# Optimization experiments

Measured on AMD Instinct MI355X. Metric: run time of the kernel, lower is better.

Reference implementation:

```python
import jax, jax.numpy as jnp
import numpy as np

NUM_HEADS = 16
HEAD_DIM = 128
MODEL_DIM = 2048
SEQ = 4096
INIT = 0.02


def setup_inputs() -> dict:
    key = jax.random.key(0)
    k1, k2, k3 = jax.random.split(key, 3)
    x = jax.random.normal(k1, (SEQ, MODEL_DIM), dtype=jnp.float32)
    w_attn = jax.random.normal(k2, (MODEL_DIM, 3 * MODEL_DIM), dtype=jnp.float32) * INIT
    b_attn = jnp.zeros((3 * MODEL_DIM,), dtype=jnp.float32)
    w_proj = jax.random.normal(k3, (MODEL_DIM, MODEL_DIM), dtype=jnp.float32) * INIT
    b_proj = jnp.zeros((MODEL_DIM,), dtype=jnp.float32)
    return {"x": x, "w_attn": w_attn, "b_attn": b_attn, "w_proj": w_proj, "b_proj": b_proj}


def reference(x, w_attn, b_attn, w_proj, b_proj):
    seq = x.shape[0]
    # fused QKV projection: [seq, 3*model_dim]
    hidden = x @ w_attn + b_attn
    q, k, v = jnp.split(hidden, 3, axis=-1)
    q = q.reshape(seq, NUM_HEADS, HEAD_DIM)
    k = k.reshape(seq, NUM_HEADS, HEAD_DIM)
    v = v.reshape(seq, NUM_HEADS, HEAD_DIM)
    q = q / jnp.sqrt(jnp.asarray(HEAD_DIM, dtype=q.dtype))
    # scores: [heads, q, k]
    scores = jnp.einsum('qhd,khd->hqk', q, k)
    causal = jnp.tril(jnp.ones((seq, seq), dtype=bool))  # mask[q, k]
    big_neg = jnp.finfo(jnp.float32).min
    scores = jnp.where(causal[None, :, :], scores, big_neg)
    pattern = jax.nn.softmax(scores, axis=-1)
    z = jnp.einsum('hqk,khd->qhd', pattern, v)
    out = z.reshape(seq, MODEL_DIM) @ w_proj + b_proj
    return out
```

## Files before the change

### kernel.cpp

```cpp
#include <hip/hip_runtime.h>
#include <hip/hip_bf16.h>
#include <stdint.h>
#include <stddef.h>

typedef __bf16 bf16_8 __attribute__((ext_vector_type(8)));
typedef __bf16 bf16_4 __attribute__((ext_vector_type(4)));
typedef float f32x4 __attribute__((ext_vector_type(4)));

#define BIG_NEG (-1e30f)
#define QSCALE (0.08838834764831845f * 1.4426950408889634f)
#define FIXMAX 16.0f

__device__ __forceinline__ void gld_lds16(const void* g, void* l) {
  __builtin_amdgcn_global_load_lds(
      (const __attribute__((address_space(1))) uint32_t*)g,
      (__attribute__((address_space(3))) uint32_t*)l, 16, 0, 0);
}

#define BAR()                      \
  do {                             \
    asm volatile("" ::: "memory"); \
    __builtin_amdgcn_s_barrier();  \
    asm volatile("" ::: "memory"); \
  } while (0)

__global__ __launch_bounds__(256) void convert_bf16(
    const float* __restrict__ in, __bf16* __restrict__ out, long long n) {
  long long i = ((long long)blockIdx.x * 256 + threadIdx.x) * 8;
  if (i + 8 > n) return;
  const float4* in4 = (const float4*)(in + i);
  float4 a = in4[0], b = in4[1];
  bf16_8 o = {(__bf16)a.x, (__bf16)a.y, (__bf16)a.z, (__bf16)a.w,
              (__bf16)b.x, (__bf16)b.y, (__bf16)b.z, (__bf16)b.w};
  *(bf16_8*)(out + i) = o;
}

__global__ __launch_bounds__(256) void transpose_cvt(
    const float* __restrict__ in, __bf16* __restrict__ out, int R, int C) {
  __shared__ __bf16 tile[32][33];
  int bx = blockIdx.x * 32;
  int by = blockIdx.y * 32;
  int tx = threadIdx.x;
  int ty = threadIdx.y;
#pragma unroll
  for (int j = 0; j < 32; j += 8)
    tile[ty + j][tx] = (__bf16)in[(size_t)(by + ty + j) * C + bx + tx];
  __syncthreads();
#pragma unroll
  for (int j = 0; j < 32; j += 8)
    out[(size_t)(bx + ty + j) * R + by + tx] = tile[tx][ty + j];
}

__global__ __launch_bounds__(512, 2) void gemm_bt256(
    const __bf16* __restrict__ A, const __bf16* __restrict__ Bt,
    const float* __restrict__ bias, __bf16* __restrict__ C0,
    __bf16* __restrict__ VT, float* __restrict__ Cf,
    int M, int N, int K, int mode) {
  __shared__ __bf16 As[2][128 * 64];
  __shared__ __bf16 Bs[2][256 * 64];

  const int t = threadIdx.x;
  const int lane = t & 63;
  const int wave = t >> 6;
  const int col = lane & 15;
  const int quad = lane >> 4;
  const int wr = wave >> 2;
  const int wc = wave & 3;
  const int m0 = blockIdx.y * 128;
  const int n0 = blockIdx.x * 256;
  const bool vswap = (mode == 1) && (n0 >= 4096);

  const int trow = t >> 3;
  const int sk = (((trow & 7) ^ (t & 7)) * 8);
  const __bf16* gA = A + (size_t)(m0 + trow) * K + sk;
  const __bf16* gB = Bt + (size_t)(n0 + trow) * K + sk;
  const int ldst = wave * 512;

  const int ar = wr * 64 + col;
  const int br = wc * 64 + col;
  const int sq0 = ((quad) ^ (col & 7)) * 8;
  const int sq1 = ((quad ^ 4) ^ (col & 7)) * 8;

  f32x4 acc[4][4];
#pragma unroll
  for (int i = 0; i < 4; i++)
#pragma unroll
    for (int j = 0; j < 4; j++) acc[i][j] = f32x4{0.f, 0.f, 0.f, 0.f};

  const int nk = K / 64;

#define STA(b, L, kk) \
  gld_lds16(gA + (size_t)(L) * 64 * K + (kk), &As[b][(L) * 4096 + ldst])
#define STB(b, L, kk) \
  gld_lds16(gB + (size_t)(L) * 64 * K + (kk), &Bs[b][(L) * 4096 + ldst])

#define RDA(c)                                                         \
  do {                                                                 \
    afp[0] = *(const bf16_8*)(&As[cb][(ar + (c) * 16) * 64 + sq0]);    \
    afp[1] = *(const bf16_8*)(&As[cb][(ar + (c) * 16) * 64 + sq1]);    \
  } while (0)

#define CL(c)                                                          \
  do {                                                                 \
    if (!vswap) {                                                      \
      _Pragma("unroll") for (int ni = 0; ni < 4; ++ni) {               \
        acc[(c)][ni] = __builtin_amdgcn_mfma_f32_16x16x32_bf16(        \
            afp[0], bfr[ni][0], acc[(c)][ni], 0, 0, 0);                \
        acc[(c)][ni] = __builtin_amdgcn_mfma_f32_16x16x32_bf16(        \
            afp[1], bfr[ni][1], acc[(c)][ni], 0, 0, 0);                \
      }                                                                \
    } else {                                                           \
      _Pragma("unroll") for (int ni = 0; ni < 4; ++ni) {               \
        acc[(c)][ni] = __builtin_amdgcn_mfma_f32_16x16x32_bf16(        \
            bfr[ni][0], afp[0], acc[(c)][ni], 0, 0, 0);                \
        acc[(c)][ni] = __builtin_amdgcn_mfma_f32_16x16x32_bf16(        \
            bfr[ni][1], afp[1], acc[(c)][ni], 0, 0, 0);                \
      }                                                                \
    }                                                                  \
  } while (0)

#define LGKM0()                                       \
  do {                                                \
    asm volatile("s_waitcnt lgkmcnt(0)" ::: "memory");\
    __builtin_amdgcn_sched_barrier(0);                \
  } while (0)

  STA(0, 0, 0); STA(0, 1, 0);
  STB(0, 0, 0); STB(0, 1, 0); STB(0, 2, 0); STB(0, 3, 0);
  STA(1, 0, 64); STA(1, 1, 64);
  STB(1, 0, 64); STB(1, 1, 64); STB(1, 2, 64); STB(1, 3, 64);
  asm volatile("s_waitcnt vmcnt(6)" ::: "memory");
  BAR();

  for (int kt = 0; kt < nk; ++kt) {
    const int cb = kt & 1;
    const int kk = (kt + 2) * 64;
    const bool st = (kt + 2) < nk;

    bf16_8 bfr[4][2], afp[2];
#pragma unroll
    for (int ni = 0; ni < 4; ++ni) {
      bfr[ni][0] = *(const bf16_8*)(&Bs[cb][(br + ni * 16) * 64 + sq0]);
      bfr[ni][1] = *(const bf16_8*)(&Bs[cb][(br + ni * 16) * 64 + sq1]);
    }
    RDA(0);
    LGKM0();
    __builtin_amdgcn_s_setprio(1);
    CL(0);
    __builtin_amdgcn_s_setprio(0);

    BAR();
    if (st) { STB(cb, 0, kk); STB(cb, 1, kk); STB(cb, 2, kk); STB(cb, 3, kk); }

    RDA(1);
    LGKM0();
    __builtin_amdgcn_s_setprio(1);
    CL(1);
    __builtin_amdgcn_s_setprio(0);

    RDA(2);
    LGKM0();
    __builtin_amdgcn_s_setprio(1);
    CL(2);
    __builtin_amdgcn_s_setprio(0);

    RDA(3);
    LGKM0();
    BAR();
    if (st) { STA(cb, 0, kk); STA(cb, 1, kk); }
    __builtin_amdgcn_sched_barrier(0);
    __builtin_amdgcn_s_setprio(1);
    CL(3);
    __builtin_amdgcn_s_setprio(0);

    if (st)
      asm volatile("s_waitcnt vmcnt(6)" ::: "memory");
    else
      asm volatile("s_waitcnt vmcnt(0)" ::: "memory");
    BAR();
  }
#undef STA
#undef STB
#undef RDA
#undef CL
#undef LGKM0

  if (mode == 0) {
#pragma unroll
    for (int mi = 0; mi < 4; mi++)
#pragma unroll
      for (int ni = 0; ni < 4; ni++) {
        int gn = n0 + wc * 64 + ni * 16 + col;
        float bv = bias[gn];
#pragma unroll
        for (int r = 0; r < 4; r++)
          Cf[(size_t)(m0 + wr * 64 + mi * 16 + quad * 4 + r) * N + gn] =
              acc[mi][ni][r] + bv;
      }
  } else if (n0 < 2048) {
#pragma unroll
    for (int mi = 0; mi < 4; mi++)
#pragma unroll
      for (int ni = 0; ni < 4; ni++) {
        int gn = n0 + wc * 64 + ni * 16 + col;
        float bv = bias[gn];
#pragma unroll
        for (int r = 0; r < 4; r++)
          C0[(size_t)(m0 + wr * 64 + mi * 16 + quad * 4 + r) * 4096 + gn] =
              (__bf16)((acc[mi][ni][r] + bv) * QSCALE);
      }
  } else if (n0 < 4096) {
#pragma unroll
    for (int mi = 0; mi < 4; mi++)
#pragma unroll
      for (int ni = 0; ni < 4; ni++) {
        int gn = n0 + wc * 64 + ni * 16 + col;
        float bv = bias[gn];
#pragma unroll
        for (int r = 0; r < 4; r++)
          C0[(size_t)(m0 + wr * 64 + mi * 16 + quad * 4 + r) * 4096 + gn] =
              (__bf16)(acc[mi][ni][r] + bv);
      }
  } else {
#pragma unroll
    for (int mi = 0; mi < 4; mi++) {
      int seq = m0 + wr * 64 + mi * 16 + col;
#pragma unroll
      for (int ni = 0; ni < 4; ni++) {
#pragma unroll
        for (int r = 0; r < 4; r++) {
          int gn = n0 + wc * 64 + ni * 16 + quad * 4 + r;
          float bv = bias[gn];
          VT[(size_t)(gn - 4096) * M + seq] = (__bf16)(acc[mi][ni][r] + bv);
        }
      }
    }
  }
}

__global__ __launch_bounds__(256, 2) void flash_attn(
    const __bf16* __restrict__ QK, const __bf16* __restrict__ VT,
    __bf16* __restrict__ Z) {
  constexpr int KS = 136;
  constexpr int VS = 72;
  constexpr int PS = 72;
  __shared__ __bf16 Ks[64 * KS];
  __shared__ __bf16 Vs[128 * VS];
  __shared__ __bf16 Ps[4 * 2 * 16 * PS];

  const int t = threadIdx.x;
  const int lane = t & 63;
  const int wave = t >> 6;
  const int col = lane & 15;
  const int quad = lane >> 4;
  const int h = blockIdx.y;
  const int ta = 31 - blockIdx.x;
  const int q0 = ta * 128;
  const int nkb = 2 * (ta + 1);

  const __bf16* kbase =
      QK + (size_t)(t >> 4) * 4096 + 2048 + h * 128 + (t & 15) * 8;
  __bf16* kdst = Ks + (t >> 4) * KS + (t & 15) * 8;
  const __bf16* vbase = VT + (size_t)(h * 128 + (t >> 3)) * 4096 + (t & 7) * 8;
  __bf16* vdst = Vs + (t >> 3) * VS + (t & 7) * 8;

  bf16_8 qf[4][2];
  {
#pragma unroll
    for (int qg = 0; qg < 2; qg++) {
      const __bf16* qp =
          QK + (size_t)(q0 + wave * 32 + qg * 16 + col) * 4096 + h * 128;
#pragma unroll
      for (int i = 0; i < 4; i++)
        qf[i][qg] = *(const bf16_8*)(qp + i * 32 + quad * 8);
    }
  }

  f32x4 z[8][2];
#pragma unroll
  for (int i = 0; i < 8; i++) {
    z[i][0] = f32x4{0.f, 0.f, 0.f, 0.f};
    z[i][1] = f32x4{0.f, 0.f, 0.f, 0.f};
  }
  float lsum[2] = {0.f, 0.f};

  bf16_8 kpre[4], vpre[4];
#pragma unroll
  for (int j = 0; j < 4; j++) {
    kpre[j] = *(const bf16_8*)(kbase + (size_t)j * 16 * 4096);
    vpre[j] = *(const bf16_8*)(vbase + (size_t)j * 32 * 4096);
  }

  __bf16* pw0 = Ps + (wave * 2 + 0) * 16 * PS;
  __bf16* pw1 = Ps + (wave * 2 + 1) * 16 * PS;

  for (int kb = 0; kb < nkb; kb++) {
    const int k0 = kb * 64;
    __syncthreads();
#pragma unroll
    for (int j = 0; j < 4; j++) {
      *(bf16_8*)(kdst + j * 16 * KS) = kpre[j];
      *(bf16_8*)(vdst + j * 32 * VS) = vpre[j];
    }
    __syncthreads();

    if (kb + 1 < nkb) {
      const __bf16* kb2 = kbase + (size_t)(k0 + 64) * 4096;
      const __bf16* vb2 = vbase + (k0 + 64);
#pragma unroll
      for (int j = 0; j < 4; j++) {
        kpre[j] = *(const bf16_8*)(kb2 + (size_t)j * 16 * 4096);
        vpre[j] = *(const bf16_8*)(vb2 + (size_t)j * 32 * 4096);
      }
    }

    f32x4 sh[4][2];
    __builtin_amdgcn_s_setprio(1);
#pragma unroll
    for (int p = 0; p < 4; p++) {
      sh[p][0] = f32x4{0.f, 0.f, 0.f, 0.f};
      sh[p][1] = f32x4{0.f, 0.f, 0.f, 0.f};
#pragma unroll
      for (int kd = 0; kd < 4; kd++) {
        bf16_8 kf =
            *(const bf16_8*)(Ks + (p * 16 + col) * KS + kd * 32 + quad * 8);
        sh[p][0] = __builtin_amdgcn_mfma_f32_16x16x32_bf16(kf, qf[kd][0],
                                                           sh[p][0], 0, 0, 0);
        sh[p][1] = __builtin_amdgcn_mfma_f32_16x16x32_bf16(kf, qf[kd][1],
                                                           sh[p][1], 0, 0, 0);
      }
    }
    __builtin_amdgcn_s_setprio(0);

    if (kb >= nkb - 2) {
#pragma unroll
      for (int qg = 0; qg < 2; qg++) {
        int qgl = q0 + wave * 32 + qg * 16 + col;
#pragma unroll
        for (int p = 0; p < 4; p++)
#pragma unroll
          for (int r = 0; r < 4; r++)
            if (k0 + p * 16 + quad * 4 + r > qgl) sh[p][qg][r] = BIG_NEG;
      }
    }

#pragma unroll
    for (int qg = 0; qg < 2; qg++) {
      __bf16* pw = qg ? pw1 : pw0;
      float rs = 0.f;
#pragma unroll
      for (int p = 0; p < 4; p++) {
        float e0 = exp2f(sh[p][qg][0] - FIXMAX);
        float e1 = exp2f(sh[p][qg][1] - FIXMAX);
        float e2 = exp2f(sh[p][qg][2] - FIXMAX);
        float e3 = exp2f(sh[p][qg][3] - FIXMAX);
        rs += (e0 + e1) + (e2 + e3);
        bf16_4 pk = {(__bf16)e0, (__bf16)e1, (__bf16)e2, (__bf16)e3};
        *(bf16_4*)(pw + col * PS + p * 16 + quad * 4) = pk;
      }
      lsum[qg] += rs;
    }

    bf16_8 pf0a = *(const bf16_8*)(pw0 + col * PS + quad * 8);
    bf16_8 pf0b = *(const bf16_8*)(pw0 + col * PS + 32 + quad * 8);
    bf16_8 pf1a = *(const bf16_8*)(pw1 + col * PS + quad * 8);
    bf16_8 pf1b = *(const bf16_8*)(pw1 + col * PS + 32 + quad * 8);

    __builtin_amdgcn_s_setprio(1);
#pragma unroll
    for (int db = 0; db < 8; db++) {
      bf16_8 vf0 = *(const bf16_8*)(Vs + (db * 16 + col) * VS + quad * 8);
      z[db][0] =
          __builtin_amdgcn_mfma_f32_16x16x32_bf16(vf0, pf0a, z[db][0], 0, 0, 0);
      z[db][1] =
          __builtin_amdgcn_mfma_f32_16x16x32_bf16(vf0, pf1a, z[db][1], 0, 0, 0);
      bf16_8 vf1 = *(const bf16_8*)(Vs + (db * 16 + col) * VS + 32 + quad * 8);
      z[db][0] =
          __builtin_amdgcn_mfma_f32_16x16x32_bf16(vf1, pf0b, z[db][0], 0, 0, 0);
      z[db][1] =
          __builtin_amdgcn_mfma_f32_16x16x32_bf16(vf1, pf1b, z[db][1], 0, 0, 0);
    }
    __builtin_amdgcn_s_setprio(0);
  }

#pragma unroll
  for (int qg = 0; qg < 2; qg++) {
    float l = lsum[qg];
    l += __shfl_xor(l, 16, 64);
    l += __shfl_xor(l, 32, 64);
    float rl = 1.f / l;
    __bf16* zrow = Z + (size_t)(q0 + wave * 32 + qg * 16 + col) * 2048 +
                   h * 128 + quad * 4;
#pragma unroll
    for (int db = 0; db < 8; db++) {
      bf16_4 o = {(__bf16)(z[db][qg][0] * rl), (__bf16)(z[db][qg][1] * rl),
                  (__bf16)(z[db][qg][2] * rl), (__bf16)(z[db][qg][3] * rl)};
      *(bf16_4*)(zrow + db * 16) = o;
    }
  }
}

extern "C" void kernel_launch(void* const* d_in, const int* in_sizes, int n_in,
                              void* d_out, int out_size, void* d_ws,
                              size_t ws_size, hipStream_t stream) {
  const float* x = (const float*)d_in[0];
  const float* w_attn = (const float*)d_in[1];
  const float* b_attn = (const float*)d_in[2];
  const float* w_proj = (const float*)d_in[3];
  const float* b_proj = (const float*)d_in[4];
  float* out = (float*)d_out;

  __bf16* ws = (__bf16*)d_ws;
  __bf16* QK = ws;
  __bf16* VT = ws + 16777216;
  __bf16* WT1 = ws + 25165824;
  __bf16* Zb = ws + 25165824;
  __bf16* WT2 = ws + 37748736;
  __bf16* xb = ws + 41943040;

  convert_bf16<<<4096, 256, 0, stream>>>(x, xb, 8388608LL);
  transpose_cvt<<<dim3(6144 / 32, 2048 / 32), dim3(32, 8), 0, stream>>>(
      w_attn, WT1, 2048, 6144);
  transpose_cvt<<<dim3(2048 / 32, 2048 / 32), dim3(32, 8), 0, stream>>>(
      w_proj, WT2, 2048, 2048);

  gemm_bt256<<<dim3(6144 / 256, 4096 / 128), 512, 0, stream>>>(
      xb, WT1, b_attn, QK, VT, nullptr, 4096, 6144, 2048, 1);

  flash_attn<<<dim3(32, 16), 256, 0, stream>>>(QK, VT, Zb);

  gemm_bt256<<<dim3(2048 / 256, 4096 / 128), 512, 0, stream>>>(
      Zb, WT2, b_proj, nullptr, nullptr, out, 4096, 2048, 2048, 0);
}
```

Measured before the change: 494.2 us.

## Make flash attention persistent with an atomic longest-first work queue

Turns the flash attention kernel into a persistent kernel. A fixed grid of 384 blocks pulls (query tile, head) tasks from a global atomic counter, ordered so that the longest causal tiles across all heads are handed out first. This is meant to balance the uneven causal workload across CUs and shrink the tail. It adds a memset, an atomic plus a barrier per task, and fewer resident blocks than the old 512-block grid.

```diff
diff --git a/kernel.cpp b/kernel.cpp
--- a/kernel.cpp
+++ b/kernel.cpp
@@ -240,32 +240,42 @@
 
 __global__ __launch_bounds__(256, 2) void flash_attn(
     const __bf16* __restrict__ QK, const __bf16* __restrict__ VT,
-    __bf16* __restrict__ Z) {
+    __bf16* __restrict__ Z, uint32_t* __restrict__ cnt) {
   constexpr int KS = 136;
   constexpr int VS = 72;
   constexpr int PS = 72;
   __shared__ __bf16 Ks[64 * KS];
   __shared__ __bf16 Vs[128 * VS];
   __shared__ __bf16 Ps[4 * 2 * 16 * PS];
+  __shared__ int s_task;
 
   const int t = threadIdx.x;
   const int lane = t & 63;
   const int wave = t >> 6;
   const int col = lane & 15;
   const int quad = lane >> 4;
-  const int h = blockIdx.y;
-  const int ta = 31 - blockIdx.x;
-  const int q0 = ta * 128;
-  const int nkb = 2 * (ta + 1);
-
-  const __bf16* kbase =
-      QK + (size_t)(t >> 4) * 4096 + 2048 + h * 128 + (t & 15) * 8;
+
   __bf16* kdst = Ks + (t >> 4) * KS + (t & 15) * 8;
-  const __bf16* vbase = VT + (size_t)(h * 128 + (t >> 3)) * 4096 + (t & 7) * 8;
   __bf16* vdst = Vs + (t >> 3) * VS + (t & 7) * 8;
-
-  bf16_8 qf[4][2];
-  {
+  __bf16* pw0 = Ps + (wave * 2 + 0) * 16 * PS;
+  __bf16* pw1 = Ps + (wave * 2 + 1) * 16 * PS;
+
+  for (;;) {
+    if (t == 0) s_task = (int)atomicAdd(cnt, 1u);
+    __syncthreads();
+    const int tau = s_task;
+    if (tau >= 512) return;
+    const int ta = 31 - (tau >> 4);
+    const int h = tau & 15;
+    const int q0 = ta * 128;
+    const int nkb = 2 * (ta + 1);
+
+    const __bf16* kbase =
+        QK + (size_t)(t >> 4) * 4096 + 2048 + h * 128 + (t & 15) * 8;
+    const __bf16* vbase =
+        VT + (size_t)(h * 128 + (t >> 3)) * 4096 + (t & 7) * 8;
+
+    bf16_8 qf[4][2];
 #pragma unroll
     for (int qg = 0; qg < 2; qg++) {
       const __bf16* qp =
@@ -274,128 +284,126 @@
       for (int i = 0; i < 4; i++)
         qf[i][qg] = *(const bf16_8*)(qp + i * 32 + quad * 8);
     }
-  }
-
-  f32x4 z[8][2];
-#pragma unroll
-  for (int i = 0; i < 8; i++) {
-    z[i][0] = f32x4{0.f, 0.f, 0.f, 0.f};
-    z[i][1] = f32x4{0.f, 0.f, 0.f, 0.f};
-  }
-  float lsum[2] = {0.f, 0.f};
-
-  bf16_8 kpre[4], vpre[4];
-#pragma unroll
-  for (int j = 0; j < 4; j++) {
-    kpre[j] = *(const bf16_8*)(kbase + (size_t)j * 16 * 4096);
-    vpre[j] = *(const bf16_8*)(vbase + (size_t)j * 32 * 4096);
-  }
-
-  __bf16* pw0 = Ps + (wave * 2 + 0) * 16 * PS;
-  __bf16* pw1 = Ps + (wave * 2 + 1) * 16 * PS;
-
-  for (int kb = 0; kb < nkb; kb++) {
-    const int k0 = kb * 64;
-    __syncthreads();
+
+    f32x4 z[8][2];
+#pragma unroll
+    for (int i = 0; i < 8; i++) {
+      z[i][0] = f32x4{0.f, 0.f, 0.f, 0.f};
+      z[i][1] = f32x4{0.f, 0.f, 0.f, 0.f};
+    }
+    float lsum[2] = {0.f, 0.f};
+
+    bf16_8 kpre[4], vpre[4];
 #pragma unroll
     for (int j = 0; j < 4; j++) {
-      *(bf16_8*)(kdst + j * 16 * KS) = kpre[j];
-      *(bf16_8*)(vdst + j * 32 * VS) = vpre[j];
-    }
-    __syncthreads();
-
-    if (kb + 1 < nkb) {
-      const __bf16* kb2 = kbase + (size_t)(k0 + 64) * 4096;
-      const __bf16* vb2 = vbase + (k0 + 64);
+      kpre[j] = *(const bf16_8*)(kbase + (size_t)j * 16 * 4096);
+      vpre[j] = *(const bf16_8*)(vbase + (size_t)j * 32 * 4096);
+    }
+
+    for (int kb = 0; kb < nkb; kb++) {
+      const int k0 = kb * 64;
+      __syncthreads();
 #pragma unroll
       for (int j = 0; j < 4; j++) {
-        kpre[j] = *(const bf16_8*)(kb2 + (size_t)j * 16 * 4096);
-        vpre[j] = *(const bf16_8*)(vb2 + (size_t)j * 32 * 4096);
-      }
-    }
-
-    f32x4 sh[4][2];
-    __builtin_amdgcn_s_setprio(1);
-#pragma unroll
-    for (int p = 0; p < 4; p++) {
-      sh[p][0] = f32x4{0.f, 0.f, 0.f, 0.f};
-      sh[p][1] = f32x4{0.f, 0.f, 0.f, 0.f};
-#pragma unroll
-      for (int kd = 0; kd < 4; kd++) {
-        bf16_8 kf =
-            *(const bf16_8*)(Ks + (p * 16 + col) * KS + kd * 32 + quad * 8);
-        sh[p][0] = __builtin_amdgcn_mfma_f32_16x16x32_bf16(kf, qf[kd][0],
-                                                           sh[p][0], 0, 0, 0);
-        sh[p][1] = __builtin_amdgcn_mfma_f32_16x16x32_bf16(kf, qf[kd][1],
-                                                           sh[p][1], 0, 0, 0);
-      }
-    }
-    __builtin_amdgcn_s_setprio(0);
-
-    if (kb >= nkb - 2) {
+        *(bf16_8*)(kdst + j * 16 * KS) = kpre[j];
+        *(bf16_8*)(vdst + j * 32 * VS) = vpre[j];
+      }
+      __syncthreads();
+
+      if (kb + 1 < nkb) {
+        const __bf16* kb2 = kbase + (size_t)(k0 + 64) * 4096;
+        const __bf16* vb2 = vbase + (k0 + 64);
+#pragma unroll
+        for (int j = 0; j < 4; j++) {
+          kpre[j] = *(const bf16_8*)(kb2 + (size_t)j * 16 * 4096);
+          vpre[j] = *(const bf16_8*)(vb2 + (size_t)j * 32 * 4096);
+        }
+      }
+
+      f32x4 sh[4][2];
+      __builtin_amdgcn_s_setprio(1);
+#pragma unroll
+      for (int p = 0; p < 4; p++) {
+        sh[p][0] = f32x4{0.f, 0.f, 0.f, 0.f};
+        sh[p][1] = f32x4{0.f, 0.f, 0.f, 0.f};
+#pragma unroll
+        for (int kd = 0; kd < 4; kd++) {
+          bf16_8 kf =
+              *(const bf16_8*)(Ks + (p * 16 + col) * KS + kd * 32 + quad * 8);
+          sh[p][0] = __builtin_amdgcn_mfma_f32_16x16x32_bf16(kf, qf[kd][0],
+                                                             sh[p][0], 0, 0, 0);
+          sh[p][1] = __builtin_amdgcn_mfma_f32_16x16x32_bf16(kf, qf[kd][1],
+                                                             sh[p][1], 0, 0, 0);
+        }
+      }
+      __builtin_amdgcn_s_setprio(0);
+
+      if (kb >= nkb - 2) {
+#pragma unroll
+        for (int qg = 0; qg < 2; qg++) {
+          int qgl = q0 + wave * 32 + qg * 16 + col;
+#pragma unroll
+          for (int p = 0; p < 4; p++)
+#pragma unroll
+            for (int r = 0; r < 4; r++)
+              if (k0 + p * 16 + quad * 4 + r > qgl) sh[p][qg][r] = BIG_NEG;
+        }
+      }
+
 #pragma unroll
       for (int qg = 0; qg < 2; qg++) {
-        int qgl = q0 + wave * 32 + qg * 16 + col;
-#pragma unroll
-        for (int p = 0; p < 4; p++)
-#pragma unroll
-          for (int r = 0; r < 4; r++)
-            if (k0 + p * 16 + quad * 4 + r > qgl) sh[p][qg][r] = BIG_NEG;
-      }
+        __bf16* pw = qg ? pw1 : pw0;
+        float rs = 0.f;
+#pragma unroll
+        for (int p = 0; p < 4; p++) {
+          float e0 = exp2f(sh[p][qg][0] - FIXMAX);
+          float e1 = exp2f(sh[p][qg][1] - FIXMAX);
+          float e2 = exp2f(sh[p][qg][2] - FIXMAX);
+          float e3 = exp2f(sh[p][qg][3] - FIXMAX);
+          rs += (e0 + e1) + (e2 + e3);
+          bf16_4 pk = {(__bf16)e0, (__bf16)e1, (__bf16)e2, (__bf16)e3};
+          *(bf16_4*)(pw + col * PS + p * 16 + quad * 4) = pk;
+        }
+        lsum[qg] += rs;
+      }
+
+      bf16_8 pf0a = *(const bf16_8*)(pw0 + col * PS + quad * 8);
+      bf16_8 pf0b = *(const bf16_8*)(pw0 + col * PS + 32 + quad * 8);
+      bf16_8 pf1a = *(const bf16_8*)(pw1 + col * PS + quad * 8);
+      bf16_8 pf1b = *(const bf16_8*)(pw1 + col * PS + 32 + quad * 8);
+
+      __builtin_amdgcn_s_setprio(1);
+#pragma unroll
+      for (int db = 0; db < 8; db++) {
+        bf16_8 vf0 = *(const bf16_8*)(Vs + (db * 16 + col) * VS + quad * 8);
+        z[db][0] = __builtin_amdgcn_mfma_f32_16x16x32_bf16(vf0, pf0a, z[db][0],
+                                                           0, 0, 0);
+        z[db][1] = __builtin_amdgcn_mfma_f32_16x16x32_bf16(vf0, pf1a, z[db][1],
+                                                           0, 0, 0);
+        bf16_8 vf1 =
+            *(const bf16_8*)(Vs + (db * 16 + col) * VS + 32 + quad * 8);
+        z[db][0] = __builtin_amdgcn_mfma_f32_16x16x32_bf16(vf1, pf0b, z[db][0],
+                                                           0, 0, 0);
+        z[db][1] = __builtin_amdgcn_mfma_f32_16x16x32_bf16(vf1, pf1b, z[db][1],
+                                                           0, 0, 0);
+      }
+      __builtin_amdgcn_s_setprio(0);
     }
 
 #pragma unroll
     for (int qg = 0; qg < 2; qg++) {
-      __bf16* pw = qg ? pw1 : pw0;
-      float rs = 0.f;
-#pragma unroll
-      for (int p = 0; p < 4; p++) {
-        float e0 = exp2f(sh[p][qg][0] - FIXMAX);
-        float e1 = exp2f(sh[p][qg][1] - FIXMAX);
-        float e2 = exp2f(sh[p][qg][2] - FIXMAX);
-        float e3 = exp2f(sh[p][qg][3] - FIXMAX);
-        rs += (e0 + e1) + (e2 + e3);
-        bf16_4 pk = {(__bf16)e0, (__bf16)e1, (__bf16)e2, (__bf16)e3};
-        *(bf16_4*)(pw + col * PS + p * 16 + quad * 4) = pk;
-      }
-      lsum[qg] += rs;
-    }
-
-    bf16_8 pf0a = *(const bf16_8*)(pw0 + col * PS + quad * 8);
-    bf16_8 pf0b = *(const bf16_8*)(pw0 + col * PS + 32 + quad * 8);
-    bf16_8 pf1a = *(const bf16_8*)(pw1 + col * PS + quad * 8);
-    bf16_8 pf1b = *(const bf16_8*)(pw1 + col * PS + 32 + quad * 8);
-
-    __builtin_amdgcn_s_setprio(1);
-#pragma unroll
-    for (int db = 0; db < 8; db++) {
-      bf16_8 vf0 = *(const bf16_8*)(Vs + (db * 16 + col) * VS + quad * 8);
-      z[db][0] =
-          __builtin_amdgcn_mfma_f32_16x16x32_bf16(vf0, pf0a, z[db][0], 0, 0, 0);
-      z[db][1] =
-          __builtin_amdgcn_mfma_f32_16x16x32_bf16(vf0, pf1a, z[db][1], 0, 0, 0);
-      bf16_8 vf1 = *(const bf16_8*)(Vs + (db * 16 + col) * VS + 32 + quad * 8);
-      z[db][0] =
-          __builtin_amdgcn_mfma_f32_16x16x32_bf16(vf1, pf0b, z[db][0], 0, 0, 0);
-      z[db][1] =
-          __builtin_amdgcn_mfma_f32_16x16x32_bf16(vf1, pf1b, z[db][1], 0, 0, 0);
-    }
-    __builtin_amdgcn_s_setprio(0);
-  }
-
-#pragma unroll
-  for (int qg = 0; qg < 2; qg++) {
-    float l = lsum[qg];
-    l += __shfl_xor(l, 16, 64);
-    l += __shfl_xor(l, 32, 64);
-    float rl = 1.f / l;
-    __bf16* zrow = Z + (size_t)(q0 + wave * 32 + qg * 16 + col) * 2048 +
-                   h * 128 + quad * 4;
-#pragma unroll
-    for (int db = 0; db < 8; db++) {
-      bf16_4 o = {(__bf16)(z[db][qg][0] * rl), (__bf16)(z[db][qg][1] * rl),
-                  (__bf16)(z[db][qg][2] * rl), (__bf16)(z[db][qg][3] * rl)};
-      *(bf16_4*)(zrow + db * 16) = o;
+      float l = lsum[qg];
+      l += __shfl_xor(l, 16, 64);
+      l += __shfl_xor(l, 32, 64);
+      float rl = 1.f / l;
+      __bf16* zrow = Z + (size_t)(q0 + wave * 32 + qg * 16 + col) * 2048 +
+                     h * 128 + quad * 4;
+#pragma unroll
+      for (int db = 0; db < 8; db++) {
+        bf16_4 o = {(__bf16)(z[db][qg][0] * rl), (__bf16)(z[db][qg][1] * rl),
+                    (__bf16)(z[db][qg][2] * rl), (__bf16)(z[db][qg][3] * rl)};
+        *(bf16_4*)(zrow + db * 16) = o;
+      }
     }
   }
 }
@@ -415,6 +423,7 @@
   __bf16* VT = ws + 16777216;
   __bf16* WT1 = ws + 25165824;
   __bf16* Zb = ws + 25165824;
+  uint32_t* cnt = (uint32_t*)(ws + 33554432);
   __bf16* WT2 = ws + 37748736;
   __bf16* xb = ws + 41943040;
 
@@ -427,7 +436,8 @@
   gemm_bt256<<<dim3(6144 / 256, 4096 / 128), 512, 0, stream>>>(
       xb, WT1, b_attn, QK, VT, nullptr, 4096, 6144, 2048, 1);
 
-  flash_attn<<<dim3(32, 16), 256, 0, stream>>>(QK, VT, Zb);
+  hipMemsetAsync((void*)cnt, 0, 4, stream);
+  flash_attn<<<dim3(384), 256, 0, stream>>>(QK, VT, Zb, cnt);
 
   gemm_bt256<<<dim3(2048 / 256, 4096 / 128), 512, 0, stream>>>(
       Zb, WT2, b_proj, nullptr, nullptr, out, 4096, 2048, 2048, 0);
```

Result: faster. 465.3 us (-5.8%).
